# Kernel tuning notes

Hardware: AMD Instinct MI355X
Metric: run time of the kernel (lower is better)

## Reference

```python
import jax, jax.numpy as jnp
import numpy as np

D_MODEL = 1024
N_HEADS = 16
D_K = D_MODEL // N_HEADS
THETA = 10000.0
SEQ = 2048
BATCH = 2


def setup_inputs() -> dict:
    key = jax.random.key(0)
    ks = jax.random.split(key, 5)
    std = (2.0 / (D_MODEL + D_MODEL)) ** 0.5
    return {
        "x": jax.random.normal(ks[0], (BATCH, SEQ, D_MODEL), dtype=jnp.float32),
        "token_positions": jnp.arange(SEQ, dtype=jnp.int64 if jax.config.jax_enable_x64 else jnp.int32),
        "wq": jax.random.normal(ks[1], (D_MODEL, D_MODEL), dtype=jnp.float32) * std,
        "wk": jax.random.normal(ks[2], (D_MODEL, D_MODEL), dtype=jnp.float32) * std,
        "wv": jax.random.normal(ks[3], (D_MODEL, D_MODEL), dtype=jnp.float32) * std,
        "wo": jax.random.normal(ks[4], (D_MODEL, D_MODEL), dtype=jnp.float32) * std,
    }


def _apply_rope(t, token_positions):
    # t: [b, h, s, d_k]; interleaved even/odd rotation (RoPE)
    k = jnp.arange(D_K // 2, dtype=t.dtype)
    inv_freq = THETA ** (-2.0 * k / D_K)                     # [d_k/2]
    angles = token_positions.astype(t.dtype)[:, None] * inv_freq  # [s, d_k/2]
    cos, sin = jnp.cos(angles), jnp.sin(angles)
    even, odd = t[..., 0::2], t[..., 1::2]
    re = even * cos - odd * sin
    ro = odd * cos + even * sin
    # re-interleave: stack last then reshape back to [..., d_k]
    return jnp.stack([re, ro], axis=-1).reshape(t.shape)


def reference(x, token_positions, wq, wk, wv, wo):
    b, s, _ = x.shape
    def proj(w):
        y = jnp.einsum("bsd,ed->bse", x, w)               # Linear: x @ W^T
        return y.reshape(b, s, N_HEADS, D_K).transpose(0, 2, 1, 3)  # [b,h,s,dk]
    q, k, v = proj(wq), proj(wk), proj(wv)
    q = _apply_rope(q, token_positions)
    k = _apply_rope(k, token_positions)
    scores = jnp.einsum("bhqd,bhkd->bhqk", q, k) / jnp.sqrt(jnp.asarray(D_K, x.dtype))
    attn = jax.nn.softmax(scores, axis=-1)
    out = jnp.einsum("bhqk,bhkd->bhqd", attn, v)          # [b,h,s,dk]
    out = out.transpose(0, 2, 1, 3).reshape(b, s, D_MODEL)
    return jnp.einsum("bsd,ed->bse", out, wo)
```

## Files before the change

### kernel.cpp

```cpp
#include <hip/hip_runtime.h>
#include <stdint.h>

typedef __bf16 bf16x8 __attribute__((ext_vector_type(8)));
typedef __bf16 bf16x2 __attribute__((ext_vector_type(2)));
typedef float f32x4 __attribute__((ext_vector_type(4)));
typedef float f32x16 __attribute__((ext_vector_type(16)));
typedef unsigned short ushort_t;
typedef unsigned int uint;
typedef uint uint4v __attribute__((ext_vector_type(4)));

#define SEQ    2048
#define DMODEL 1024
#define NHEAD  16
#define DKH    64
#define NBATCH 2
#define MROWS  (NBATCH*SEQ)
#define LOG2E  1.44269504088896340736f

__device__ __forceinline__ uint pk2(float a, float b) {
  bf16x2 t; t[0] = (__bf16)a; t[1] = (__bf16)b;
  return __builtin_bit_cast(uint, t);
}
__device__ __forceinline__ ushort_t b1(float a) {
  return __builtin_bit_cast(ushort_t, (__bf16)a);
}
__device__ __forceinline__ float fexp2(float x) {
#if __has_builtin(__builtin_amdgcn_exp2f)
  return __builtin_amdgcn_exp2f(x);
#else
  return exp2f(x);
#endif
}

__device__ __forceinline__ void gload16(const void* g, void* l) {
  __builtin_amdgcn_global_load_lds(
      (const __attribute__((address_space(1))) void*)g,
      (__attribute__((address_space(3))) void*)l, 16, 0, 0);
}

__device__ __forceinline__ f32x4 mfma16(bf16x8 a, bf16x8 b, f32x4 c) {
  return __builtin_amdgcn_mfma_f32_16x16x32_bf16(a, b, c, 0, 0, 0);
}
__device__ __forceinline__ f32x16 mfma32(bf16x8 a, bf16x8 b, f32x16 c) {
  return __builtin_amdgcn_mfma_f32_32x32x16_bf16(a, b, c, 0, 0, 0);
}

__global__ __launch_bounds__(256) void cvt_all(
    const float* __restrict__ x, const float* __restrict__ wq,
    const float* __restrict__ wk, const float* __restrict__ wv,
    const float* __restrict__ wo, const int* __restrict__ tokpos,
    uint2* __restrict__ out, float2* __restrict__ tab)
{
  int b = blockIdx.x;
  if (b >= 8192) {
    int t = (b - 8192) * 256 + threadIdx.x;
    int s = t >> 5, k = t & 31;
    double inv = pow(10000.0, -(double)(2 * k) / 64.0);
    double ang = (double)tokpos[s] * inv;
    tab[t] = make_float2((float)cos(ang), (float)sin(ang));
    return;
  }
  const float4* src; uint2* dst; int i;
  if (b < 4096) {
    i = b * 256 + threadIdx.x; src = (const float4*)x; dst = out;
  } else {
    int s = (b - 4096) >> 10;
    i = ((b - 4096) & 1023) * 256 + threadIdx.x;
    src = (const float4*)(s == 0 ? wq : s == 1 ? wk : s == 2 ? wv : wo);
    dst = out + (size_t)1048576 + (size_t)s * 262144;
  }
  float4 v = src[i];
  uint2 r; r.x = pk2(v.x, v.y); r.y = pk2(v.z, v.w);
  dst[i] = r;
}

__global__ __launch_bounds__(256) void gemm_nt(
    const ushort_t* __restrict__ A, const ushort_t* __restrict__ W,
    const float2* __restrict__ tab,
    ushort_t* __restrict__ Qo, ushort_t* __restrict__ Ko, ushort_t* __restrict__ Vo,
    float* __restrict__ outf, int fused, int nbx)
{
  __shared__ ushort_t lA[2][128 * 64];
  __shared__ ushort_t lB[2][128 * 64];
  const int tid = threadIdx.x;
  const int lin = blockIdx.y * nbx + blockIdx.x;
  const int nwg = nbx * gridDim.y;
  const int n = (lin & 7) * (nwg >> 3) + (lin >> 3);
  const int vbx = n % nbx, vby = n / nbx;
  const int w = tid >> 6, l = tid & 63, lo = l & 15, hi = l >> 4;
  const int wr = (w >> 1) * 64, wc = (w & 1) * 64;
  const char* Ab = (const char*)A + (size_t)vby * 128 * 2048;
  const char* Bb = (const char*)W + (size_t)vbx * 128 * 2048;
  f32x4 acc[4][4] = {};

  const int o0 = w * 1024 + l * 16;
  const int r0 = o0 >> 7;
  const int us = ((o0 >> 4) & 7) ^ (r0 & 7);
  const char* ap = Ab + (size_t)r0 * 2048 + us * 16;
  const char* bp = Bb + (size_t)r0 * 2048 + us * 16;

  auto stage = [&](char* dA, char* dB, const char* aq, const char* bq) {
    #pragma unroll
    for (int i = 0; i < 4; ++i) {
      gload16(aq + i * 65536, dA + w * 1024 + i * 4096);
      gload16(bq + i * 65536, dB + w * 1024 + i * 4096);
    }
  };
  auto comp = [&](const ushort_t* lAb, const ushort_t* lBb) {
    #pragma unroll
    for (int c = 0; c < 2; ++c) {
      bf16x8 af[4], wf[4];
      #pragma unroll
      for (int m = 0; m < 4; ++m) {
        int row = wr + m * 16 + lo;
        af[m] = *(const bf16x8*)((const char*)lAb + row * 128 + ((c * 64 + hi * 16) ^ ((row & 7) << 4)));
      }
      #pragma unroll
      for (int n2 = 0; n2 < 4; ++n2) {
        int row = wc + n2 * 16 + lo;
        wf[n2] = *(const bf16x8*)((const char*)lBb + row * 128 + ((c * 64 + hi * 16) ^ ((row & 7) << 4)));
      }
      #pragma unroll
      for (int m = 0; m < 4; ++m)
        #pragma unroll
        for (int n2 = 0; n2 < 4; ++n2)
          acc[m][n2] = mfma16(af[m], wf[n2], acc[m][n2]);
    }
  };

  stage((char*)lA[0], (char*)lB[0], ap, bp); ap += 128; bp += 128;
  #pragma unroll 1
  for (int it = 0; it < 8; ++it) {
    stage((char*)lA[1], (char*)lB[1], ap, bp); ap += 128; bp += 128;
    asm volatile("s_waitcnt vmcnt(8)" ::: "memory");
    __builtin_amdgcn_s_barrier();
    asm volatile("" ::: "memory");
    comp(lA[0], lB[0]);
    __builtin_amdgcn_s_barrier();
    asm volatile("" ::: "memory");
    if (it < 7) {
      stage((char*)lA[0], (char*)lB[0], ap, bp); ap += 128; bp += 128;
      asm volatile("s_waitcnt vmcnt(8)" ::: "memory");
    } else {
      asm volatile("s_waitcnt vmcnt(0)" ::: "memory");
    }
    __builtin_amdgcn_s_barrier();
    asm volatile("" ::: "memory");
    comp(lA[1], lB[1]);
    __builtin_amdgcn_s_barrier();
    asm volatile("" ::: "memory");
  }

  const int mode = fused ? (vbx >> 3) : 3;
  const int colblk = fused ? (vbx & 7) : vbx;
  const int rowbase = vby * 128 + wr + hi * 4;
  const int colbase = colblk * 128 + wc + lo;

  if (mode == 3) {
    #pragma unroll
    for (int m = 0; m < 4; ++m)
      #pragma unroll
      for (int n2 = 0; n2 < 4; ++n2) {
        int e = colbase + n2 * 16;
        #pragma unroll
        for (int r = 0; r < 4; ++r) {
          int row = rowbase + m * 16 + r;
          outf[(size_t)row * 1024 + e] = acc[m][n2][r];
        }
      }
    return;
  }
  if (mode == 2) {
    #pragma unroll
    for (int m = 0; m < 4; ++m) {
      int row0 = rowbase + m * 16;
      int b = row0 >> 11, s = row0 & 2047;
      int b2 = (s >> 2) & 3;
      int sp = (s & ~12) | ((b2 & 1) << 3) | ((b2 >> 1) << 2);
      #pragma unroll
      for (int n2 = 0; n2 < 4; ++n2) {
        int e = colbase + n2 * 16;
        int h = e >> 6, dk = e & 63;
        uint2 pk;
        pk.x = pk2(acc[m][n2][0], acc[m][n2][1]);
        pk.y = pk2(acc[m][n2][2], acc[m][n2][3]);
        *(uint2*)(Vo + ((size_t)((b * NHEAD + h) * DKH + dk) * SEQ + sp)) = pk;
      }
    }
    return;
  }
  ushort_t* outb = (mode == 0) ? Qo : Ko;
  const float qscale = (mode == 0) ? (0.125f * LOG2E) : 1.0f;
  #pragma unroll
  for (int m = 0; m < 4; ++m) {
    #pragma unroll
    for (int n2 = 0; n2 < 4; ++n2) {
      int e = colbase + n2 * 16;
      int h = e >> 6, dk = e & 63, kf = dk >> 1;
      float sgn = (e & 1) ? 1.0f : -1.0f;
      #pragma unroll
      for (int r = 0; r < 4; ++r) {
        int row = rowbase + m * 16 + r;
        int s = row & 2047, b = row >> 11;
        float2 cs = tab[s * 32 + kf];
        float v = acc[m][n2][r];
        float p = __shfl_xor(v, 1, 64);
        float res = (v * cs.x + sgn * p * cs.y) * qscale;
        outb[((size_t)((b * NHEAD + h) * SEQ + s)) * DKH + dk] = b1(res);
      }
    }
  }
}

__global__ __launch_bounds__(256) void attn_fwd(
    const ushort_t* __restrict__ Qg, const ushort_t* __restrict__ Kg,
    const ushort_t* __restrict__ VTg, ushort_t* __restrict__ attn)
{
  __shared__ char lds[67584];
  const int tid = threadIdx.x;
  const int w = tid >> 6, l = tid & 63;
  const int q31 = l & 31, hf = l >> 5, s7 = l & 7;
  const int lin = blockIdx.y * gridDim.x + blockIdx.x;
  const int n = (lin & 7) * 128 + (lin >> 3);
  const int bh = n >> 5;
  const int q0 = (n & 31) * 64;
  const char* Kb = (const char*)Kg + (size_t)bh * 2048 * 128;
  const char* Vb = (const char*)VTg + (size_t)bh * 64 * 4096;

  bf16x8 qreg[2][4];
  #pragma unroll
  for (int qb = 0; qb < 2; ++qb) {
    const ushort_t* qp = Qg + ((size_t)bh * 2048 + q0 + qb * 32 + q31) * 64 + hf * 8;
    #pragma unroll
    for (int c = 0; c < 4; ++c) qreg[qb][c] = *(const bf16x8*)(qp + c * 16);
  }

  f32x16 accO[2][2] = {};
  float lsum[2] = {0.f, 0.f};

  char* wlds = lds + w * 16384;
  const char* ra[4];
  #pragma unroll
  for (int c = 0; c < 4; ++c)
    ra[c] = wlds + q31 * 128 + ((c * 32 + hf * 16) ^ (s7 << 4));

  const int usw = (l & 7) ^ (l >> 3);
  const int kb0 = w * 512;
  const char* kst = Kb + (size_t)(kb0 + (l >> 3)) * 128 + usw * 16;
  const char* vst = Vb + (size_t)((l >> 3) + (usw >> 2) * 32) * 4096
                       + (size_t)kb0 * 2 + (usw & 3) * 16;

  auto stageT = [&](int slot) {
    char* sp = wlds + slot;
    #pragma unroll
    for (int i = 0; i < 4; ++i)
      gload16(kst + i * 1024, sp + i * 1024 + l * 16);
    #pragma unroll
    for (int i = 0; i < 4; ++i)
      gload16(vst + i * 32768, sp + 4096 + i * 1024 + l * 16);
    kst += 4096; vst += 64;
  };

  stageT(0);
  #pragma unroll 2
  for (int t = 0; t < 16; ++t) {
    const int bo = (t & 1) * 8192;
    asm volatile("s_waitcnt vmcnt(0)" ::: "memory");
    bf16x8 kf[4], vA[2], vB[2];
    #pragma unroll
    for (int c = 0; c < 4; ++c)
      kf[c] = *(const bf16x8*)(ra[c] + bo);
    vA[0] = *(const bf16x8*)(ra[0] + bo + 4096);
    vB[0] = *(const bf16x8*)(ra[2] + bo + 4096);
    vA[1] = *(const bf16x8*)(ra[1] + bo + 4096);
    vB[1] = *(const bf16x8*)(ra[3] + bo + 4096);
    asm volatile("s_waitcnt lgkmcnt(0)" ::: "memory");
    if (t < 15) stageT(((t + 1) & 1) * 8192);
    f32x16 s0 = {}, s1 = {};
    __builtin_amdgcn_s_setprio(1);
    #pragma unroll
    for (int c = 0; c < 4; ++c) {
      s0 = mfma32(kf[c], qreg[0][c], s0);
      s1 = mfma32(kf[c], qreg[1][c], s1);
    }
    __builtin_amdgcn_s_setprio(0);
    float p0[16], p1[16];
    float t0 = 0.f, t1 = 0.f;
    #pragma unroll
    for (int r = 0; r < 16; ++r) { p0[r] = fexp2(s0[r]); t0 += p0[r]; }
    #pragma unroll
    for (int r = 0; r < 16; ++r) { p1[r] = fexp2(s1[r]); t1 += p1[r]; }
    lsum[0] += t0; lsum[1] += t1;
    #pragma unroll
    for (int kcl = 0; kcl < 2; ++kcl) {
      const float* a0 = p0 + kcl * 8;
      const float* a1 = p1 + kcl * 8;
      uint4v u0 = { pk2(a0[0], a0[1]), pk2(a0[2], a0[3]),
                    pk2(a0[4], a0[5]), pk2(a0[6], a0[7]) };
      uint4v u1 = { pk2(a1[0], a1[1]), pk2(a1[2], a1[3]),
                    pk2(a1[4], a1[5]), pk2(a1[6], a1[7]) };
      bf16x8 pb0 = __builtin_bit_cast(bf16x8, u0);
      bf16x8 pb1 = __builtin_bit_cast(bf16x8, u1);
      __builtin_amdgcn_s_setprio(1);
      accO[0][0] = mfma32(vA[kcl], pb0, accO[0][0]);
      accO[0][1] = mfma32(vB[kcl], pb0, accO[0][1]);
      accO[1][0] = mfma32(vA[kcl], pb1, accO[1][0]);
      accO[1][1] = mfma32(vB[kcl], pb1, accO[1][1]);
      __builtin_amdgcn_s_setprio(0);
    }
  }

  __syncthreads();
  #pragma unroll
  for (int qb = 0; qb < 2; ++qb)
    #pragma unroll
    for (int db = 0; db < 2; ++db)
      #pragma unroll
      for (int c2 = 0; c2 < 4; ++c2) {
        int j = qb * 8 + db * 4 + c2;
        f32x4 v = { accO[qb][db][c2 * 4 + 0], accO[qb][db][c2 * 4 + 1],
                    accO[qb][db][c2 * 4 + 2], accO[qb][db][c2 * 4 + 3] };
        *(f32x4*)(lds + w * 16384 + j * 1024 + l * 16) = v;
      }
  *(float2*)(lds + 65536 + w * 512 + l * 8) = make_float2(lsum[0], lsum[1]);
  __syncthreads();

  float lt0 = 0.f, lt1 = 0.f;
  #pragma unroll
  for (int wp = 0; wp < 4; ++wp) {
    float2 lo = *(const float2*)(lds + 65536 + wp * 512 + l * 8);
    lt0 += lo.x; lt1 += lo.y;
  }
  lt0 += __shfl_xor(lt0, 32, 64);
  lt1 += __shfl_xor(lt1, 32, 64);
  float inv0 = 1.0f / lt0, inv1 = 1.0f / lt1;
  int b = bh >> 4, head = bh & 15;
  #pragma unroll
  for (int jj = 0; jj < 4; ++jj) {
    int j = w * 4 + jj;
    int qb = j >> 3, db = (j >> 2) & 1, c2 = j & 3;
    f32x4 v = {0.f, 0.f, 0.f, 0.f};
    #pragma unroll
    for (int wp = 0; wp < 4; ++wp) {
      f32x4 u = *(const f32x4*)(lds + wp * 16384 + j * 1024 + l * 16);
      v[0] += u[0]; v[1] += u[1]; v[2] += u[2]; v[3] += u[3];
    }
    float inv = qb ? inv1 : inv0;
    int d0 = db * 32 + c2 * 8 + hf * 4;
    ushort_t* op = attn + (size_t)(b * 2048 + q0 + qb * 32 + q31) * 1024 + head * 64;
    uint2 pk;
    pk.x = pk2(v[0] * inv, v[1] * inv);
    pk.y = pk2(v[2] * inv, v[3] * inv);
    *(uint2*)(op + d0) = pk;
  }
}

extern "C" void kernel_launch(void* const* d_in, const int* in_sizes, int n_in,
                              void* d_out, int out_size, void* d_ws, size_t ws_size,
                              hipStream_t stream) {
  const float* x  = (const float*)d_in[0];
  const int* tok  = (const int*)d_in[1];
  const float* wq = (const float*)d_in[2];
  const float* wk = (const float*)d_in[3];
  const float* wv = (const float*)d_in[4];
  const float* wo = (const float*)d_in[5];
  float* out = (float*)d_out;
  char* ws = (char*)d_ws;

  size_t off = 0;
  float2* tab = (float2*)(ws + off); off += (size_t)SEQ * 32 * sizeof(float2);
  ushort_t* xb  = (ushort_t*)(ws + off); off += (size_t)MROWS * DMODEL * 2;
  ushort_t* wqkv = (ushort_t*)(ws + off); off += (size_t)3 * DMODEL * DMODEL * 2;
  ushort_t* wob = (ushort_t*)(ws + off); off += (size_t)DMODEL * DMODEL * 2;
  ushort_t* Qg  = (ushort_t*)(ws + off); off += (size_t)MROWS * DMODEL * 2;
  ushort_t* Kg  = (ushort_t*)(ws + off); off += (size_t)MROWS * DMODEL * 2;
  ushort_t* VTg = (ushort_t*)(ws + off); off += (size_t)MROWS * DMODEL * 2;
  ushort_t* attnb = xb;
  if (ws_size < off) return;

  cvt_all<<<8448, 256, 0, stream>>>(x, wq, wk, wv, wo, tok, (uint2*)xb, tab);

  gemm_nt<<<dim3(24, 32), 256, 0, stream>>>(xb, wqkv, tab, Qg, Kg, VTg, nullptr, 1, 24);

  attn_fwd<<<dim3(SEQ / 64, NBATCH * NHEAD), 256, 0, stream>>>(Qg, Kg, VTg, attnb);

  gemm_nt<<<dim3(8, 32), 256, 0, stream>>>(attnb, wob, nullptr, nullptr, nullptr, nullptr, out, 0, 8);
}
```

Measured before the change: 119.5 us.

## Add 256x256-tile 8-wave QKV GEMM with staggered LDS prefetch pipeline

```diff
diff --git a/kernel.cpp b/kernel.cpp
--- a/kernel.cpp
+++ b/kernel.cpp
@@ -44,6 +44,8 @@
 __device__ __forceinline__ f32x16 mfma32(bf16x8 a, bf16x8 b, f32x16 c) {
   return __builtin_amdgcn_mfma_f32_32x32x16_bf16(a, b, c, 0, 0, 0);
 }
+
+#define BARRIER() do { __builtin_amdgcn_s_barrier(); asm volatile("" ::: "memory"); } while (0)
 
 __global__ __launch_bounds__(256) void cvt_all(
     const float* __restrict__ x, const float* __restrict__ wq,
@@ -74,11 +76,188 @@
   dst[i] = r;
 }
 
+__global__ __launch_bounds__(512, 1) void gemm_qkv(
+    const ushort_t* __restrict__ A, const ushort_t* __restrict__ W,
+    const float2* __restrict__ tab,
+    ushort_t* __restrict__ Qo, ushort_t* __restrict__ Ko, ushort_t* __restrict__ Vo)
+{
+  __shared__ char lds[131072];
+  const int tid = threadIdx.x;
+  const int w = tid >> 6, l = tid & 63;
+  const int wm = w >> 2, wn = w & 3;
+  const int lo = l & 15, hi = l >> 4;
+  const int lin = blockIdx.y * 12 + blockIdx.x;
+  const int vn = (lin & 7) * 24 + (lin >> 3);
+  const int vbx = vn % 12, vby = vn / 12;
+  const char* Ab = (const char*)A + (size_t)vby * 256 * 2048;
+  const char* Bb = (const char*)W + (size_t)vbx * 256 * 2048;
+
+  const int sr = tid >> 3;
+  const int us = (tid & 7) ^ (sr & 7);
+  const char* aSrc = Ab + (size_t)sr * 2048 + us * 16;
+  const char* bSrc = Bb + (size_t)sr * 2048 + us * 16;
+
+  f32x4 acc[8][4] = {};
+
+  auto stg = [&](char* dst, const char* src) {
+    gload16(src,          dst + tid * 16);
+    gload16(src + 131072, dst + 8192 + tid * 16);
+  };
+
+  stg(lds,                 aSrc);
+  stg(lds + 16384,         aSrc + 262144);
+  stg(lds + 32768,         bSrc);
+  stg(lds + 49152,         bSrc + 262144);
+  stg(lds + 98304,         bSrc + 128);
+  stg(lds + 114688,        bSrc + 128 + 262144);
+  asm volatile("s_waitcnt vmcnt(4)" ::: "memory");
+  BARRIER();
+
+  #pragma unroll 1
+  for (int t = 0; t < 16; ++t) {
+    const int b = t & 1;
+    const char* lA = lds + b * 65536;
+    const char* lB = lA + 32768;
+    char* nA = lds + (b ^ 1) * 65536;
+    char* nB = (char*)lB;
+    bf16x8 af[4][2], wf[4][2];
+
+    #pragma unroll
+    for (int m = 0; m < 4; ++m) {
+      int row = wm * 128 + m * 16 + lo;
+      const char* base = lA + row * 128;
+      int sw = (row & 7) << 4;
+      af[m][0] = *(const bf16x8*)(base + ((hi * 16) ^ sw));
+      af[m][1] = *(const bf16x8*)(base + ((64 + hi * 16) ^ sw));
+    }
+    #pragma unroll
+    for (int j = 0; j < 2; ++j) {
+      int row = wn * 64 + j * 16 + lo;
+      const char* base = lB + row * 128;
+      int sw = (row & 7) << 4;
+      wf[j][0] = *(const bf16x8*)(base + ((hi * 16) ^ sw));
+      wf[j][1] = *(const bf16x8*)(base + ((64 + hi * 16) ^ sw));
+    }
+    if (t < 15) stg(nA, aSrc + (t + 1) * 128);
+    BARRIER();
+    __builtin_amdgcn_s_setprio(1);
+    #pragma unroll
+    for (int m = 0; m < 4; ++m)
+      #pragma unroll
+      for (int n2 = 0; n2 < 2; ++n2) {
+        acc[m][n2] = mfma16(af[m][0], wf[n2][0], acc[m][n2]);
+        acc[m][n2] = mfma16(af[m][1], wf[n2][1], acc[m][n2]);
+      }
+    __builtin_amdgcn_s_setprio(0);
+    BARRIER();
+
+    #pragma unroll
+    for (int j = 2; j < 4; ++j) {
+      int row = wn * 64 + j * 16 + lo;
+      const char* base = lB + row * 128;
+      int sw = (row & 7) << 4;
+      wf[j][0] = *(const bf16x8*)(base + ((hi * 16) ^ sw));
+      wf[j][1] = *(const bf16x8*)(base + ((64 + hi * 16) ^ sw));
+    }
+    if (t < 15) stg(nA + 16384, aSrc + (t + 1) * 128 + 262144);
+    BARRIER();
+    __builtin_amdgcn_s_setprio(1);
+    #pragma unroll
+    for (int m = 0; m < 4; ++m)
+      #pragma unroll
+      for (int n2 = 2; n2 < 4; ++n2) {
+        acc[m][n2] = mfma16(af[m][0], wf[n2][0], acc[m][n2]);
+        acc[m][n2] = mfma16(af[m][1], wf[n2][1], acc[m][n2]);
+      }
+    __builtin_amdgcn_s_setprio(0);
+    BARRIER();
+
+    #pragma unroll
+    for (int m = 0; m < 4; ++m) {
+      int row = wm * 128 + 64 + m * 16 + lo;
+      const char* base = lA + row * 128;
+      int sw = (row & 7) << 4;
+      af[m][0] = *(const bf16x8*)(base + ((hi * 16) ^ sw));
+      af[m][1] = *(const bf16x8*)(base + ((64 + hi * 16) ^ sw));
+    }
+    if (t < 14) stg(nB, bSrc + (t + 2) * 128);
+    BARRIER();
+    __builtin_amdgcn_s_setprio(1);
+    #pragma unroll
+    for (int m = 0; m < 4; ++m)
+      #pragma unroll
+      for (int n2 = 0; n2 < 2; ++n2) {
+        acc[4 + m][n2] = mfma16(af[m][0], wf[n2][0], acc[4 + m][n2]);
+        acc[4 + m][n2] = mfma16(af[m][1], wf[n2][1], acc[4 + m][n2]);
+      }
+    __builtin_amdgcn_s_setprio(0);
+    BARRIER();
+
+    if (t < 14) stg(nB + 16384, bSrc + (t + 2) * 128 + 262144);
+    BARRIER();
+    __builtin_amdgcn_s_setprio(1);
+    #pragma unroll
+    for (int m = 0; m < 4; ++m)
+      #pragma unroll
+      for (int n2 = 2; n2 < 4; ++n2) {
+        acc[4 + m][n2] = mfma16(af[m][0], wf[n2][0], acc[4 + m][n2]);
+        acc[4 + m][n2] = mfma16(af[m][1], wf[n2][1], acc[4 + m][n2]);
+      }
+    __builtin_amdgcn_s_setprio(0);
+    if (t < 14)       asm volatile("s_waitcnt vmcnt(4)" ::: "memory");
+    else if (t == 14) asm volatile("s_waitcnt vmcnt(0)" ::: "memory");
+    BARRIER();
+  }
+
+  const int mode = vbx >> 2;
+  const int colbase = (vbx & 3) * 256 + wn * 64 + lo;
+  const int rowb0 = vby * 256 + wm * 128 + hi * 4;
+
+  if (mode == 2) {
+    #pragma unroll
+    for (int i = 0; i < 8; ++i) {
+      int row0 = rowb0 + i * 16;
+      int bb = row0 >> 11, s = row0 & 2047;
+      int b2 = (s >> 2) & 3;
+      int sp = (s & ~12) | ((b2 & 1) << 3) | ((b2 >> 1) << 2);
+      #pragma unroll
+      for (int n2 = 0; n2 < 4; ++n2) {
+        int e = colbase + n2 * 16;
+        int h = e >> 6, dk = e & 63;
+        uint2 pk;
+        pk.x = pk2(acc[i][n2][0], acc[i][n2][1]);
+        pk.y = pk2(acc[i][n2][2], acc[i][n2][3]);
+        *(uint2*)(Vo + ((size_t)((bb * NHEAD + h) * DKH + dk) * SEQ + sp)) = pk;
+      }
+    }
+    return;
+  }
+  ushort_t* outb = (mode == 0) ? Qo : Ko;
+  const float qscale = (mode == 0) ? (0.125f * LOG2E) : 1.0f;
+  #pragma unroll
+  for (int i = 0; i < 8; ++i) {
+    #pragma unroll
+    for (int n2 = 0; n2 < 4; ++n2) {
+      int e = colbase + n2 * 16;
+      int h = e >> 6, dk = e & 63, kf = dk >> 1;
+      float sgn = (e & 1) ? 1.0f : -1.0f;
+      #pragma unroll
+      for (int r = 0; r < 4; ++r) {
+        int row = rowb0 + i * 16 + r;
+        int s = row & 2047, bb = row >> 11;
+        float2 cs = tab[s * 32 + kf];
+        float v = acc[i][n2][r];
+        float p = __shfl_xor(v, 1, 64);
+        float res = (v * cs.x + sgn * p * cs.y) * qscale;
+        outb[((size_t)((bb * NHEAD + h) * SEQ + s)) * DKH + dk] = b1(res);
+      }
+    }
+  }
+}
+
 __global__ __launch_bounds__(256) void gemm_nt(
     const ushort_t* __restrict__ A, const ushort_t* __restrict__ W,
-    const float2* __restrict__ tab,
-    ushort_t* __restrict__ Qo, ushort_t* __restrict__ Ko, ushort_t* __restrict__ Vo,
-    float* __restrict__ outf, int fused, int nbx)
+    float* __restrict__ outf, int nbx)
 {
   __shared__ ushort_t lA[2][128 * 64];
   __shared__ ushort_t lB[2][128 * 64];
@@ -133,83 +312,33 @@
   for (int it = 0; it < 8; ++it) {
     stage((char*)lA[1], (char*)lB[1], ap, bp); ap += 128; bp += 128;
     asm volatile("s_waitcnt vmcnt(8)" ::: "memory");
-    __builtin_amdgcn_s_barrier();
-    asm volatile("" ::: "memory");
+    BARRIER();
     comp(lA[0], lB[0]);
-    __builtin_amdgcn_s_barrier();
-    asm volatile("" ::: "memory");
+    BARRIER();
     if (it < 7) {
       stage((char*)lA[0], (char*)lB[0], ap, bp); ap += 128; bp += 128;
       asm volatile("s_waitcnt vmcnt(8)" ::: "memory");
     } else {
       asm volatile("s_waitcnt vmcnt(0)" ::: "memory");
     }
-    __builtin_amdgcn_s_barrier();
-    asm volatile("" ::: "memory");
+    BARRIER();
     comp(lA[1], lB[1]);
-    __builtin_amdgcn_s_barrier();
-    asm volatile("" ::: "memory");
-  }
-
-  const int mode = fused ? (vbx >> 3) : 3;
-  const int colblk = fused ? (vbx & 7) : vbx;
+    BARRIER();
+  }
+
   const int rowbase = vby * 128 + wr + hi * 4;
-  const int colbase = colblk * 128 + wc + lo;
-
-  if (mode == 3) {
-    #pragma unroll
-    for (int m = 0; m < 4; ++m)
-      #pragma unroll
-      for (int n2 = 0; n2 < 4; ++n2) {
-        int e = colbase + n2 * 16;
-        #pragma unroll
-        for (int r = 0; r < 4; ++r) {
-          int row = rowbase + m * 16 + r;
-          outf[(size_t)row * 1024 + e] = acc[m][n2][r];
-        }
-      }
-    return;
-  }
-  if (mode == 2) {
-    #pragma unroll
-    for (int m = 0; m < 4; ++m) {
-      int row0 = rowbase + m * 16;
-      int b = row0 >> 11, s = row0 & 2047;
-      int b2 = (s >> 2) & 3;
-      int sp = (s & ~12) | ((b2 & 1) << 3) | ((b2 >> 1) << 2);
-      #pragma unroll
-      for (int n2 = 0; n2 < 4; ++n2) {
-        int e = colbase + n2 * 16;
-        int h = e >> 6, dk = e & 63;
-        uint2 pk;
-        pk.x = pk2(acc[m][n2][0], acc[m][n2][1]);
-        pk.y = pk2(acc[m][n2][2], acc[m][n2][3]);
-        *(uint2*)(Vo + ((size_t)((b * NHEAD + h) * DKH + dk) * SEQ + sp)) = pk;
-      }
-    }
-    return;
-  }
-  ushort_t* outb = (mode == 0) ? Qo : Ko;
-  const float qscale = (mode == 0) ? (0.125f * LOG2E) : 1.0f;
-  #pragma unroll
-  for (int m = 0; m < 4; ++m) {
+  const int colbase = vbx * 128 + wc + lo;
+  #pragma unroll
+  for (int m = 0; m < 4; ++m)
     #pragma unroll
     for (int n2 = 0; n2 < 4; ++n2) {
       int e = colbase + n2 * 16;
-      int h = e >> 6, dk = e & 63, kf = dk >> 1;
-      float sgn = (e & 1) ? 1.0f : -1.0f;
       #pragma unroll
       for (int r = 0; r < 4; ++r) {
         int row = rowbase + m * 16 + r;
-        int s = row & 2047, b = row >> 11;
-        float2 cs = tab[s * 32 + kf];
-        float v = acc[m][n2][r];
-        float p = __shfl_xor(v, 1, 64);
-        float res = (v * cs.x + sgn * p * cs.y) * qscale;
-        outb[((size_t)((b * NHEAD + h) * SEQ + s)) * DKH + dk] = b1(res);
-      }
-    }
-  }
+        outf[(size_t)row * 1024 + e] = acc[m][n2][r];
+      }
+    }
 }
 
 __global__ __launch_bounds__(256) void attn_fwd(
@@ -328,8 +457,8 @@
   float lt0 = 0.f, lt1 = 0.f;
   #pragma unroll
   for (int wp = 0; wp < 4; ++wp) {
-    float2 lo = *(const float2*)(lds + 65536 + wp * 512 + l * 8);
-    lt0 += lo.x; lt1 += lo.y;
+    float2 lo2 = *(const float2*)(lds + 65536 + wp * 512 + l * 8);
+    lt0 += lo2.x; lt1 += lo2.y;
   }
   lt0 += __shfl_xor(lt0, 32, 64);
   lt1 += __shfl_xor(lt1, 32, 64);
@@ -380,9 +509,9 @@
 
   cvt_all<<<8448, 256, 0, stream>>>(x, wq, wk, wv, wo, tok, (uint2*)xb, tab);
 
-  gemm_nt<<<dim3(24, 32), 256, 0, stream>>>(xb, wqkv, tab, Qg, Kg, VTg, nullptr, 1, 24);
+  gemm_qkv<<<dim3(12, 16), 512, 0, stream>>>(xb, wqkv, tab, Qg, Kg, VTg);
 
   attn_fwd<<<dim3(SEQ / 64, NBATCH * NHEAD), 256, 0, stream>>>(Qg, Kg, VTg, attnb);
 
-  gemm_nt<<<dim3(8, 32), 256, 0, stream>>>(attnb, wob, nullptr, nullptr, nullptr, nullptr, out, 0, 8);
-}
+  gemm_nt<<<dim3(8, 32), 256, 0, stream>>>(attnb, wob, out, 8);
+}
```

Result: no change. 118.1 us (-1.2%).
